# Kernel optimization log

Measured on AMD Instinct MI355X. Metric: run time of the kernel, lower is better.

## Reference

```python
import jax, jax.numpy as jnp
import numpy as np

K = 9  # 3x3 kernel field

def _conv(x, w, b, pad):
    out = jax.lax.conv_general_dilated(x, w, (1, 1), ((pad, pad), (pad, pad)),
                                       dimension_numbers=('NCHW', 'OIHW', 'NCHW'))
    return out + b[None, :, None, None]

def _conv_transpose(x, w, b):
    # torch ConvTranspose2d(k=3, stride=2, padding=1, output_padding=1); w: [Cin, Cout, 3, 3]
    wk = jnp.flip(jnp.transpose(w, (1, 0, 2, 3)), axis=(2, 3))  # [Cout, Cin, 3, 3]
    out = jax.lax.conv_general_dilated(x, wk, (1, 1), ((1, 2), (1, 2)),
                                       lhs_dilation=(2, 2),
                                       dimension_numbers=('NCHW', 'OIHW', 'NCHW'))
    return out + b[None, :, None, None]

def _modulated_deform_conv(x, offset, mask, w, b):
    # x: [B,C,H,W], offset: [B,2K,H,W] (y,x interleaved per kernel point, row-major),
    # mask: [B,K,H,W], w: [O,C,3,3]; stride=1, pad=1, dilation=1
    B, C, H, W = x.shape
    O = w.shape[0]
    off = offset.reshape(B, K, 2, H, W)
    ky, kx = jnp.meshgrid(jnp.arange(3), jnp.arange(3), indexing='ij')
    base_y = (jnp.arange(H)[None, :, None] - 1 + ky.reshape(K, 1, 1)).astype(x.dtype)  # [K,H,1]
    base_x = (jnp.arange(W)[None, None, :] - 1 + kx.reshape(K, 1, 1)).astype(x.dtype)  # [K,1,W]
    py = off[:, :, 0] + base_y[None]  # [B,K,H,W]
    px = off[:, :, 1] + base_x[None]
    y0 = jnp.floor(py); x0 = jnp.floor(px)
    wy = py - y0; wx = px - x0
    y0i = y0.astype(jnp.int32); x0i = x0.astype(jnp.int32)
    flat = x.reshape(B, C, H * W)

    def gather(yi, xi):
        valid = ((yi >= 0) & (yi < H) & (xi >= 0) & (xi < W)).astype(x.dtype)
        idx = jnp.clip(yi, 0, H - 1) * W + jnp.clip(xi, 0, W - 1)  # [B,K,H,W]
        g = jax.vmap(lambda im, ix: im[:, ix])(flat, idx.reshape(B, -1))  # [B,C,K*H*W]
        return g.reshape(B, C, K, H, W) * valid[:, None]

    v = (gather(y0i, x0i)         * ((1 - wy) * (1 - wx))[:, None]
       + gather(y0i, x0i + 1)     * ((1 - wy) * wx)[:, None]
       + gather(y0i + 1, x0i)     * (wy * (1 - wx))[:, None]
       + gather(y0i + 1, x0i + 1) * (wy * wx)[:, None])
    v = v * mask[:, None]  # modulation
    out = jnp.einsum('bckhw,ock->bohw', v, w.reshape(O, C, K))
    return out + b[None, :, None, None]

def setup_inputs() -> dict:
    key = jax.random.key(0)
    ks = jax.random.split(key, 8)
    B, Cin, Cout, H, W = 4, 128, 64, 64, 64
    return {
        'high_feature': jax.random.normal(ks[0], (B, Cin, H, W), jnp.float32),
        'low_feature': jax.random.normal(ks[1], (B, Cout, 2 * H, 2 * W), jnp.float32),
        'w_up': jax.random.normal(ks[2], (Cin, Cout, 3, 3), jnp.float32) * 0.03,
        'b_up': jnp.zeros((Cout,), jnp.float32),
        'w_off': jax.random.normal(ks[3], (3 * K, 2 * Cout, 3, 3), jnp.float32) * 0.02,
        'b_off': jnp.zeros((3 * K,), jnp.float32),
        'w_align': jax.random.normal(ks[4], (Cout, Cout, 3, 3), jnp.float32) * 0.04,
        'b_align': jnp.zeros((Cout,), jnp.float32),
    }

def reference(high_feature, low_feature, w_up, b_up, w_off, b_off, w_align, b_align):
    up = _conv_transpose(high_feature, w_up, b_up)            # [B,Cout,2H,2W]
    fo = _conv(jnp.concatenate([up, low_feature], axis=1), w_off, b_off, 1)
    offset, mask = fo[:, :2 * K], fo[:, 2 * K:]
    mask = 2.0 * jax.nn.sigmoid(mask)
    aligned = _modulated_deform_conv(up, offset, mask, w_align, b_align)
    aligned = jnp.where(aligned >= 0, aligned, 0.2 * aligned)  # LeakyReLU(0.2)
    return jnp.concatenate([aligned, low_feature], axis=1)
```

## Files before the change

kernel.cpp:

```cpp
#include <hip/hip_runtime.h>
#include <math.h>

namespace {
constexpr int B   = 4;
constexpr int CIN = 128;
constexpr int CO  = 64;
constexpr int HF  = 64;
constexpr int HO  = 128;
constexpr int HW  = HO * HO;
constexpr int NOFF = 27;

constexpr size_t UPB  = 0;
constexpr size_t LOB  = UPB + (size_t)B * HW * CO / 2;
constexpr size_t HBF  = LOB + (size_t)B * HW * CO / 2;
constexpr size_t WFRG = HBF + (size_t)B * HF * HF * CIN / 2;
constexpr size_t WFUP = WFRG + (size_t)(4 * 18 * 64 * 8) / 2;
constexpr size_t WFOF = WFUP + (size_t)(9 * 4 * 4 * 64 * 8) / 2;
}

using short8 = __attribute__((ext_vector_type(8))) short;
using f32x4  = __attribute__((ext_vector_type(4))) float;

__device__ __forceinline__ unsigned short f2bf(float f) {
  unsigned u = __float_as_uint(f);
  u += 0x7fffu + ((u >> 16) & 1u);
  return (unsigned short)(u >> 16);
}

__global__ void k_repack(const float* __restrict__ wup, const float* __restrict__ woff,
                         const float* __restrict__ wal, float* __restrict__ ws) {
  int i = blockIdx.x * 256 + threadIdx.x;
  if (i < 4 * 18 * 64 * 8) {
    int j = i & 7; int t2 = i >> 3;
    int lane = t2 & 63; int t3 = t2 >> 6;
    int kb = t3 % 18; int w = t3 / 18;
    int tap = kb >> 1;
    int c = (kb & 1) * 32 + ((lane >> 4) << 3) + j;
    int o = (w << 4) + (lane & 15);
    unsigned short* wfrag = (unsigned short*)(ws + WFRG);
    wfrag[i] = f2bf(wal[((size_t)o * CO + c) * 9 + tap]);
  }
  if (i < 9 * 4 * 4 * 64 * 8) {
    int j = i & 7; int lane = (i >> 3) & 63; int w = (i >> 9) & 3;
    int ch = (i >> 11) & 3; int rr = i >> 13;
    int c = ch * 32 + ((lane >> 4) << 3) + j;
    int o = w * 16 + (lane & 15);
    unsigned short* wfup = (unsigned short*)(ws + WFUP);
    wfup[i] = f2bf(wup[((size_t)c * CO + o) * 9 + rr]);
  }
  if (i < 9 * 4 * 2 * 64 * 8) {
    int j = i & 7; int lane = (i >> 3) & 63; int nt = (i >> 9) & 1;
    int kc = (i >> 10) & 3; int tap = i >> 12;
    int c = kc * 32 + ((lane >> 4) << 3) + j;
    int o = nt * 16 + (lane & 15);
    float v = 0.f;
    if (o < NOFF) v = woff[(((size_t)o * 2 * CO + c) * 3 + tap / 3) * 3 + (tap % 3)];
    unsigned short* wfo = (unsigned short*)(ws + WFOF);
    wfo[i] = f2bf(v);
  }
}

__global__ __launch_bounds__(256) void k_cvt(const float* __restrict__ high,
                                             float* __restrict__ ws) {
  __shared__ unsigned short tl[32][66];
  unsigned short* hbf = (unsigned short*)(ws + HBF);
  const int t = threadIdx.x;
  const int y = blockIdx.x, b = blockIdx.y;
  const int x = t & 63, clb = t >> 6;

  for (int c0 = 0; c0 < CIN; c0 += 32) {
    __syncthreads();
#pragma unroll
    for (int k = 0; k < 8; ++k) {
      int cl = clb * 8 + k;
      float v = high[(((size_t)b * CIN + c0 + cl) * HF + y) * HF + x];
      tl[cl][x] = f2bf(v);
    }
    __syncthreads();
    int px = t >> 2, cg = t & 3;
    ushort4 a, bb;
    a.x = tl[cg * 8 + 0][px]; a.y = tl[cg * 8 + 1][px];
    a.z = tl[cg * 8 + 2][px]; a.w = tl[cg * 8 + 3][px];
    bb.x = tl[cg * 8 + 4][px]; bb.y = tl[cg * 8 + 5][px];
    bb.z = tl[cg * 8 + 6][px]; bb.w = tl[cg * 8 + 7][px];
    unsigned short* dst = hbf + (((size_t)b * HF + y) * HF + px) * CIN + c0 + cg * 8;
    *(ushort4*)(dst) = a;
    *(ushort4*)(dst + 4) = bb;
  }
}

__global__ __launch_bounds__(256) void k_cvt2(const float* __restrict__ low,
                                              float* __restrict__ out,
                                              float* __restrict__ ws) {
  __shared__ unsigned short tl[64][130];
  unsigned short* lob = (unsigned short*)(ws + LOB);
  const int t = threadIdx.x;
  const int y = blockIdx.x, b = blockIdx.y;

#pragma unroll
  for (int it = 0; it < 8; ++it) {
    int i = it * 256 + t;
    int c = i >> 5, xi = (i & 31) * 4;
    float4 v = *(const float4*)(low + (((size_t)b * CO + c) * HO + y) * HO + xi);
    *(float4*)(out + (((size_t)b * 2 * CO + CO + c) * HO + y) * HO + xi) = v;
    tl[c][xi + 0] = f2bf(v.x); tl[c][xi + 1] = f2bf(v.y);
    tl[c][xi + 2] = f2bf(v.z); tl[c][xi + 3] = f2bf(v.w);
  }
  __syncthreads();
#pragma unroll
  for (int it = 0; it < 4; ++it) {
    int i = it * 256 + t;
    int x = i >> 3, cg = i & 7;
    unsigned rw[4];
#pragma unroll
    for (int p = 0; p < 4; ++p)
      rw[p] = (unsigned)tl[cg * 8 + 2 * p][x] | ((unsigned)tl[cg * 8 + 2 * p + 1][x] << 16);
    *(uint4*)(lob + (((size_t)b * HO + y) * HO + x) * CO + cg * 8) =
        make_uint4(rw[0], rw[1], rw[2], rw[3]);
  }
}

union SmemUp {
  unsigned short At[2][4][85][8];
  float accs[4][16][65];
};

__global__ __launch_bounds__(256) void k_up(const float* __restrict__ bup,
                                            float* __restrict__ ws) {
  __shared__ SmemUp sm;
  const unsigned short* hbf = (const unsigned short*)(ws + HBF);
  const uint4* wfu = (const uint4*)(ws + WFUP);
  unsigned short* upb = (unsigned short*)(ws + UPB);

  const int t    = threadIdx.x;
  const int lane = t & 63;
  const int oq   = __builtin_amdgcn_readfirstlane(t >> 6);
  const int z    = blockIdx.z;
  const int b    = z >> 2;
  const int pyv  = (z >> 1) & 1, pxv = z & 1;
  const int ty   = blockIdx.y * 4;
  const int tx   = blockIdx.x * 16;
  const int nty  = pyv + 1, ntx = pxv + 1;

  uint4 s0, s1;
  const int pxA = t >> 2, cgA = t & 3;
  const int i2 = t + 256, pxB = i2 >> 2, cgB = i2 & 3;

  auto load_chunk = [&](int c0) {
    {
      int gy = ty + pxA / 17, gx = tx + pxA % 17;
      s0 = make_uint4(0, 0, 0, 0);
      if (gy < HF && gx < HF)
        s0 = *(const uint4*)(hbf + (((size_t)b * HF + gy) * HF + gx) * CIN + c0 + cgA * 8);
    }
    s1 = make_uint4(0, 0, 0, 0);
    if (pxB < 85) {
      int gy = ty + pxB / 17, gx = tx + pxB % 17;
      if (gy < HF && gx < HF)
        s1 = *(const uint4*)(hbf + (((size_t)b * HF + gy) * HF + gx) * CIN + c0 + cgB * 8);
    }
  };
  auto write_chunk = [&](int buf) {
    *(uint4*)&sm.At[buf][cgA][pxA][0] = s0;
    if (pxB < 85) *(uint4*)&sm.At[buf][cgB][pxB][0] = s1;
  };

  f32x4 acc[4];
#pragma unroll
  for (int mt = 0; mt < 4; ++mt) acc[mt] = {0.f, 0.f, 0.f, 0.f};

  load_chunk(0);
  write_chunk(0);
  __syncthreads();

  union Cvt { uint4 u; short8 s; };
  int buf = 0;
#pragma unroll 1
  for (int ch = 0; ch < 4; ++ch) {
    if (ch < 3) load_chunk((ch + 1) * 32);
#pragma unroll
    for (int ti = 0; ti < 2; ++ti) {
      if (ti < nty) {
#pragma unroll
        for (int tj = 0; tj < 2; ++tj) {
          if (tj < ntx) {
            int ryA = pyv ? 2 - 2 * ti : 1;
            int rxA = pxv ? 2 - 2 * tj : 1;
            int rr = ryA * 3 + rxA;
            Cvt bw; bw.u = wfu[(((size_t)rr * 4 + ch) * 4 + oq) * 64 + lane];
#pragma unroll
            for (int mt = 0; mt < 4; ++mt) {
              Cvt av;
              av.u = *(const uint4*)&sm.At[buf][lane >> 4][(mt + ti) * 17 + (lane & 15) + tj][0];
              acc[mt] = __builtin_amdgcn_mfma_f32_16x16x32_bf16(av.s, bw.s, acc[mt], 0, 0, 0);
            }
          }
        }
      }
    }
    if (ch < 3) write_chunk(buf ^ 1);
    __syncthreads();
    buf ^= 1;
  }

#pragma unroll
  for (int mt = 0; mt < 4; ++mt)
#pragma unroll
    for (int r = 0; r < 4; ++r)
      sm.accs[oq][lane & 15][mt * 16 + (lane >> 4) * 4 + r] = acc[mt][r];
  __syncthreads();

  const int yo = 2 * (ty + (lane >> 4)) + pyv;
  const int xo = 2 * (tx + (lane & 15)) + pxv;
  unsigned short* dst = upb + (((size_t)b * HO + yo) * HO + xo) * CO + oq * 16;
  unsigned rw[8];
#pragma unroll
  for (int p = 0; p < 8; ++p) {
    float v0 = sm.accs[oq][2 * p][lane] + bup[oq * 16 + 2 * p];
    float v1 = sm.accs[oq][2 * p + 1][lane] + bup[oq * 16 + 2 * p + 1];
    rw[p] = (unsigned)f2bf(v0) | ((unsigned)f2bf(v1) << 16);
  }
  *(uint4*)dst = make_uint4(rw[0], rw[1], rw[2], rw[3]);
  *(uint4*)(dst + 8) = make_uint4(rw[4], rw[5], rw[6], rw[7]);
}

__global__ __launch_bounds__(256) void k_offdcn(const float* __restrict__ boff,
                                                const float* __restrict__ bal,
                                                float* __restrict__ out,
                                                const float* __restrict__ ws) {
  __shared__ float smem[9088];
  unsigned short* us_in = (unsigned short*)smem;
  float* fo_raw = smem;
  float* prm = smem + 2112;
  unsigned short* us_vt = (unsigned short*)(smem + 4992);

  const unsigned short* upb = (const unsigned short*)(ws + UPB);
  const unsigned short* lob = (const unsigned short*)(ws + LOB);
  const uint4* wfo = (const uint4*)(ws + WFOF);
  const uint4* wf  = (const uint4*)(ws + WFRG);

  const int t = threadIdx.x;
  const int lane = t & 63;
  const int w = __builtin_amdgcn_readfirstlane(t >> 6);
  const int mh = w >> 1, nt = w & 1;
  const int oq = w;
  const int b = blockIdx.z;
  const int tY = blockIdx.y * 4, tX = blockIdx.x * 16;
  const unsigned short* upB = upb + (size_t)b * HW * CO;

  union Cvt { uint4 u; short8 s; };

  for (int i = t; i < 16 * 108; i += 256) {
    int px = i >> 4, cg = i & 15;
    int gy = tY - 1 + px / 18, gx = tX - 1 + px % 18;
    uint4 v = make_uint4(0, 0, 0, 0);
    if (gy >= 0 && gy < HO && gx >= 0 && gx < HO) {
      const unsigned short* src =
          (cg < 8 ? upb : lob) + (((size_t)b * HO + gy) * HO + gx) * CO + (cg & 7) * 8;
      v = *(const uint4*)src;
    }
    *(uint4*)&us_in[((size_t)cg * 108 + px) * 8] = v;
  }
  __syncthreads();

  f32x4 acc2[2];
  acc2[0] = {0.f, 0.f, 0.f, 0.f}; acc2[1] = {0.f, 0.f, 0.f, 0.f};
#pragma unroll 1
  for (int tap = 0; tap < 9; ++tap) {
    int ky = tap / 3, kx = tap % 3;
#pragma unroll
    for (int kc = 0; kc < 4; ++kc) {
      Cvt bw; bw.u = wfo[(((size_t)tap * 4 + kc) * 2 + nt) * 64 + lane];
#pragma unroll
      for (int mt = 0; mt < 2; ++mt) {
        int sy = mh * 2 + mt;
        Cvt av;
        av.u = *(const uint4*)&us_in[(((size_t)(kc * 4 + (lane >> 4))) * 108 +
                                      (sy + ky) * 18 + (lane & 15) + kx) * 8];
        acc2[mt] = __builtin_amdgcn_mfma_f32_16x16x32_bf16(av.s, bw.s, acc2[mt], 0, 0, 0);
      }
    }
  }
  __syncthreads();

#pragma unroll
  for (int mt = 0; mt < 2; ++mt)
#pragma unroll
    for (int r = 0; r < 4; ++r)
      fo_raw[(nt * 16 + (lane & 15)) * 66 + mh * 32 + mt * 16 + (lane >> 4) * 4 + r] =
          acc2[mt][r];
  __syncthreads();

  for (int i = t; i < 9 * 64; i += 256) {
    int k = i >> 6, px = i & 63;
    int y = tY + (px >> 4), x = tX + (px & 15);
    float offy = fo_raw[(2 * k) * 66 + px] + boff[2 * k];
    float offx = fo_raw[(2 * k + 1) * 66 + px] + boff[2 * k + 1];
    float m = 2.f / (1.f + expf(-(fo_raw[(18 + k) * 66 + px] + boff[18 + k])));
    float pyf = offy + (float)(y - 1 + k / 3);
    float pxf = offx + (float)(x - 1 + k % 3);
    float y0f = floorf(pyf), x0f = floorf(pxf);
    float wy = pyf - y0f, wx = pxf - x0f;
    int y0 = (int)y0f, x0 = (int)x0f;
    int y1 = y0 + 1, x1 = x0 + 1;
    float vy0 = (y0 >= 0 && y0 < HO) ? m : 0.f;
    float vy1 = (y1 >= 0 && y1 < HO) ? m : 0.f;
    float vx0 = (x0 >= 0 && x0 < HO) ? 1.f : 0.f;
    float vx1 = (x1 >= 0 && x1 < HO) ? 1.f : 0.f;
    float* pr = prm + ((size_t)k * 64 + px) * 5;
    pr[0] = (1.f - wy) * (1.f - wx) * vy0 * vx0;
    pr[1] = (1.f - wy) * wx * vy0 * vx1;
    pr[2] = wy * (1.f - wx) * vy1 * vx0;
    pr[3] = wy * wx * vy1 * vx1;
    int cy0 = min(max(y0, 0), HO - 1), cy1 = min(max(y1, 0), HO - 1);
    int cx0 = min(max(x0, 0), HO - 1), cx1 = min(max(x1, 0), HO - 1);
    unsigned pc = (unsigned)cy0 | ((unsigned)cy1 << 8) |
                  ((unsigned)cx0 << 16) | ((unsigned)cx1 << 24);
    pr[4] = __uint_as_float(pc);
  }
  __syncthreads();

  uint4 u00[2], u01[2], u10[2], u11[2];

  auto issue = [&](int k) {
#pragma unroll
    for (int it = 0; it < 2; ++it) {
      int j = it * 256 + t;
      int q = j & 7, px = j >> 3;
      unsigned pc = __float_as_uint(prm[((size_t)k * 64 + px) * 5 + 4]);
      int cy0 = pc & 255, cy1 = (pc >> 8) & 255, cx0 = (pc >> 16) & 255, cx1 = pc >> 24;
      const unsigned short* base = upB + q * 8;
      u00[it] = *(const uint4*)(base + (size_t)(cy0 * HO + cx0) * CO);
      u01[it] = *(const uint4*)(base + (size_t)(cy0 * HO + cx1) * CO);
      u10[it] = *(const uint4*)(base + (size_t)(cy1 * HO + cx0) * CO);
      u11[it] = *(const uint4*)(base + (size_t)(cy1 * HO + cx1) * CO);
    }
  };

  auto combine = [&](int k, int buf) {
#pragma unroll
    for (int it = 0; it < 2; ++it) {
      int j = it * 256 + t;
      int q = j & 7, px = j >> 3;
      const float* pr = prm + ((size_t)k * 64 + px) * 5;
      float w0 = pr[0], w1 = pr[1], w2 = pr[2], w3 = pr[3];
      unsigned a0[4] = {u00[it].x, u00[it].y, u00[it].z, u00[it].w};
      unsigned a1[4] = {u01[it].x, u01[it].y, u01[it].z, u01[it].w};
      unsigned a2[4] = {u10[it].x, u10[it].y, u10[it].z, u10[it].w};
      unsigned a3[4] = {u11[it].x, u11[it].y, u11[it].z, u11[it].w};
      unsigned rw[4];
#pragma unroll
      for (int p = 0; p < 4; ++p) {
        float l0 = __uint_as_float(a0[p] << 16), h0 = __uint_as_float(a0[p] & 0xffff0000u);
        float l1 = __uint_as_float(a1[p] << 16), h1 = __uint_as_float(a1[p] & 0xffff0000u);
        float l2 = __uint_as_float(a2[p] << 16), h2 = __uint_as_float(a2[p] & 0xffff0000u);
        float l3 = __uint_as_float(a3[p] << 16), h3 = __uint_as_float(a3[p] & 0xffff0000u);
        float vlo = fmaf(w0, l0, fmaf(w1, l1, fmaf(w2, l2, w3 * l3)));
        float vhi = fmaf(w0, h0, fmaf(w1, h1, fmaf(w2, h2, w3 * h3)));
        rw[p] = (unsigned)f2bf(vlo) | ((unsigned)f2bf(vhi) << 16);
      }
      *(uint4*)&us_vt[(((size_t)buf * 8 + q) * 64 + px) * 8] = make_uint4(rw[0], rw[1], rw[2], rw[3]);
    }
  };

  f32x4 acc[4];
#pragma unroll
  for (int mt = 0; mt < 4; ++mt) acc[mt] = {0.f, 0.f, 0.f, 0.f};

  uint4 bw0 = wf[(oq * 18 + 0) * 64 + lane];
  uint4 bw1 = wf[(oq * 18 + 1) * 64 + lane];
  uint4 bn0, bn1;

  issue(0);
  combine(0, 0);
  __syncthreads();

  int buf = 0;
#pragma unroll 1
  for (int k = 0; k < 9; ++k) {
    if (k < 8) {
      issue(k + 1);
      bn0 = wf[(oq * 18 + 2 * k + 2) * 64 + lane];
      bn1 = wf[(oq * 18 + 2 * k + 3) * 64 + lane];
    }
#pragma unroll
    for (int kb2 = 0; kb2 < 2; ++kb2) {
      Cvt bfr; bfr.u = kb2 ? bw1 : bw0;
#pragma unroll
      for (int mt = 0; mt < 4; ++mt) {
        Cvt av;
        av.u = *(const uint4*)&us_vt[(((size_t)buf * 8 + kb2 * 4 + (lane >> 4)) * 64 +
                                      mt * 16 + (lane & 15)) * 8];
        acc[mt] = __builtin_amdgcn_mfma_f32_16x16x32_bf16(av.s, bfr.s, acc[mt], 0, 0, 0);
      }
    }
    if (k < 8) combine(k + 1, buf ^ 1);
    __syncthreads();
    bw0 = bn0; bw1 = bn1;
    buf ^= 1;
  }

  float* accs = smem;
#pragma unroll
  for (int mt = 0; mt < 4; ++mt)
#pragma unroll
    for (int r = 0; r < 4; ++r)
      accs[((size_t)oq * 16 + (lane & 15)) * 65 + mt * 16 + (lane >> 4) * 4 + r] = acc[mt][r];
  __syncthreads();

  const int y = tY + (lane >> 4), x = tX + (lane & 15);
  float* ob = out + (size_t)b * 2 * CO * HW + (size_t)y * HO + x;
#pragma unroll
  for (int ol = 0; ol < 16; ++ol) {
    int o = oq * 16 + ol;
    float v = accs[((size_t)oq * 16 + ol) * 65 + lane] + bal[o];
    v = (v >= 0.f) ? v : 0.2f * v;
    ob[(size_t)o * HW] = v;
  }
}

extern "C" void kernel_launch(void* const* d_in, const int* in_sizes, int n_in,
                              void* d_out, int out_size, void* d_ws, size_t ws_size,
                              hipStream_t stream) {
  const float* high = (const float*)d_in[0];
  const float* low  = (const float*)d_in[1];
  const float* wup  = (const float*)d_in[2];
  const float* bup  = (const float*)d_in[3];
  const float* woff = (const float*)d_in[4];
  const float* boff = (const float*)d_in[5];
  const float* wal  = (const float*)d_in[6];
  const float* bal  = (const float*)d_in[7];
  float* out = (float*)d_out;
  float* ws  = (float*)d_ws;

  k_repack<<<dim3(288), dim3(256), 0, stream>>>(wup, woff, wal, ws);
  k_cvt<<<dim3(HF, B), dim3(256), 0, stream>>>(high, ws);
  k_cvt2<<<dim3(HO, B), dim3(256), 0, stream>>>(low, out, ws);
  k_up<<<dim3(4, 16, B * 4), dim3(256), 0, stream>>>(bup, ws);
  k_offdcn<<<dim3(8, 32, B), dim3(256), 0, stream>>>(boff, bal, out, ws);
}
```

Before: 71.28 us.

## Merge prep kernels, swizzle block order for XCD locality, pack DCN params in bf16

Folds the weight repack and both layout-conversion kernels into one launch, with the work split by block-index ranges. This removes two kernel launches and the gaps between them. k_up and k_offdcn now use a 1D grid whose block index is remapped so that neighbouring tiles land on the same XCD (orig&7 interleave), which should improve L2 reuse. The bilinear weights in the deform-conv shared-memory parameters are packed as bf16 pairs, shrinking LDS from 9088 to 7936 floats to allow higher occupancy, at some cost in weight precision.

```diff
diff --git a/kernel.cpp b/kernel.cpp
--- a/kernel.cpp
+++ b/kernel.cpp
@@ -27,96 +27,103 @@
   return (unsigned short)(u >> 16);
 }
 
-__global__ void k_repack(const float* __restrict__ wup, const float* __restrict__ woff,
-                         const float* __restrict__ wal, float* __restrict__ ws) {
-  int i = blockIdx.x * 256 + threadIdx.x;
-  if (i < 4 * 18 * 64 * 8) {
-    int j = i & 7; int t2 = i >> 3;
-    int lane = t2 & 63; int t3 = t2 >> 6;
-    int kb = t3 % 18; int w = t3 / 18;
-    int tap = kb >> 1;
-    int c = (kb & 1) * 32 + ((lane >> 4) << 3) + j;
-    int o = (w << 4) + (lane & 15);
-    unsigned short* wfrag = (unsigned short*)(ws + WFRG);
-    wfrag[i] = f2bf(wal[((size_t)o * CO + c) * 9 + tap]);
-  }
-  if (i < 9 * 4 * 4 * 64 * 8) {
-    int j = i & 7; int lane = (i >> 3) & 63; int w = (i >> 9) & 3;
-    int ch = (i >> 11) & 3; int rr = i >> 13;
-    int c = ch * 32 + ((lane >> 4) << 3) + j;
-    int o = w * 16 + (lane & 15);
-    unsigned short* wfup = (unsigned short*)(ws + WFUP);
-    wfup[i] = f2bf(wup[((size_t)c * CO + o) * 9 + rr]);
-  }
-  if (i < 9 * 4 * 2 * 64 * 8) {
-    int j = i & 7; int lane = (i >> 3) & 63; int nt = (i >> 9) & 1;
-    int kc = (i >> 10) & 3; int tap = i >> 12;
-    int c = kc * 32 + ((lane >> 4) << 3) + j;
-    int o = nt * 16 + (lane & 15);
-    float v = 0.f;
-    if (o < NOFF) v = woff[(((size_t)o * 2 * CO + c) * 3 + tap / 3) * 3 + (tap % 3)];
-    unsigned short* wfo = (unsigned short*)(ws + WFOF);
-    wfo[i] = f2bf(v);
-  }
-}
-
-__global__ __launch_bounds__(256) void k_cvt(const float* __restrict__ high,
-                                             float* __restrict__ ws) {
-  __shared__ unsigned short tl[32][66];
-  unsigned short* hbf = (unsigned short*)(ws + HBF);
-  const int t = threadIdx.x;
-  const int y = blockIdx.x, b = blockIdx.y;
-  const int x = t & 63, clb = t >> 6;
-
-  for (int c0 = 0; c0 < CIN; c0 += 32) {
-    __syncthreads();
-#pragma unroll
-    for (int k = 0; k < 8; ++k) {
-      int cl = clb * 8 + k;
-      float v = high[(((size_t)b * CIN + c0 + cl) * HF + y) * HF + x];
-      tl[cl][x] = f2bf(v);
-    }
-    __syncthreads();
-    int px = t >> 2, cg = t & 3;
-    ushort4 a, bb;
-    a.x = tl[cg * 8 + 0][px]; a.y = tl[cg * 8 + 1][px];
-    a.z = tl[cg * 8 + 2][px]; a.w = tl[cg * 8 + 3][px];
-    bb.x = tl[cg * 8 + 4][px]; bb.y = tl[cg * 8 + 5][px];
-    bb.z = tl[cg * 8 + 6][px]; bb.w = tl[cg * 8 + 7][px];
-    unsigned short* dst = hbf + (((size_t)b * HF + y) * HF + px) * CIN + c0 + cg * 8;
-    *(ushort4*)(dst) = a;
-    *(ushort4*)(dst + 4) = bb;
-  }
-}
-
-__global__ __launch_bounds__(256) void k_cvt2(const float* __restrict__ low,
+__global__ __launch_bounds__(256) void k_prep(const float* __restrict__ high,
+                                              const float* __restrict__ low,
+                                              const float* __restrict__ wup,
+                                              const float* __restrict__ woff,
+                                              const float* __restrict__ wal,
                                               float* __restrict__ out,
                                               float* __restrict__ ws) {
   __shared__ unsigned short tl[64][130];
-  unsigned short* lob = (unsigned short*)(ws + LOB);
+  const int bid = blockIdx.x;
   const int t = threadIdx.x;
-  const int y = blockIdx.x, b = blockIdx.y;
-
-#pragma unroll
-  for (int it = 0; it < 8; ++it) {
-    int i = it * 256 + t;
-    int c = i >> 5, xi = (i & 31) * 4;
-    float4 v = *(const float4*)(low + (((size_t)b * CO + c) * HO + y) * HO + xi);
-    *(float4*)(out + (((size_t)b * 2 * CO + CO + c) * HO + y) * HO + xi) = v;
-    tl[c][xi + 0] = f2bf(v.x); tl[c][xi + 1] = f2bf(v.y);
-    tl[c][xi + 2] = f2bf(v.z); tl[c][xi + 3] = f2bf(v.w);
-  }
-  __syncthreads();
-#pragma unroll
-  for (int it = 0; it < 4; ++it) {
-    int i = it * 256 + t;
-    int x = i >> 3, cg = i & 7;
-    unsigned rw[4];
-#pragma unroll
-    for (int p = 0; p < 4; ++p)
-      rw[p] = (unsigned)tl[cg * 8 + 2 * p][x] | ((unsigned)tl[cg * 8 + 2 * p + 1][x] << 16);
-    *(uint4*)(lob + (((size_t)b * HO + y) * HO + x) * CO + cg * 8) =
-        make_uint4(rw[0], rw[1], rw[2], rw[3]);
+
+  if (bid < 288) {
+    int i = bid * 256 + t;
+    if (i < 4 * 18 * 64 * 8) {
+      int j = i & 7; int t2 = i >> 3;
+      int lane = t2 & 63; int t3 = t2 >> 6;
+      int kb = t3 % 18; int w = t3 / 18;
+      int tap = kb >> 1;
+      int c = (kb & 1) * 32 + ((lane >> 4) << 3) + j;
+      int o = (w << 4) + (lane & 15);
+      unsigned short* wfrag = (unsigned short*)(ws + WFRG);
+      wfrag[i] = f2bf(wal[((size_t)o * CO + c) * 9 + tap]);
+    }
+    if (i < 9 * 4 * 4 * 64 * 8) {
+      int j = i & 7; int lane = (i >> 3) & 63; int w = (i >> 9) & 3;
+      int ch = (i >> 11) & 3; int rr = i >> 13;
+      int c = ch * 32 + ((lane >> 4) << 3) + j;
+      int o = w * 16 + (lane & 15);
+      unsigned short* wfup = (unsigned short*)(ws + WFUP);
+      wfup[i] = f2bf(wup[((size_t)c * CO + o) * 9 + rr]);
+    }
+    if (i < 9 * 4 * 2 * 64 * 8) {
+      int j = i & 7; int lane = (i >> 3) & 63; int nt = (i >> 9) & 1;
+      int kc = (i >> 10) & 3; int tap = i >> 12;
+      int c = kc * 32 + ((lane >> 4) << 3) + j;
+      int o = nt * 16 + (lane & 15);
+      float v = 0.f;
+      if (o < NOFF) v = woff[(((size_t)o * 2 * CO + c) * 3 + tap / 3) * 3 + (tap % 3)];
+      unsigned short* wfo = (unsigned short*)(ws + WFOF);
+      wfo[i] = f2bf(v);
+    }
+    return;
+  }
+
+  if (bid < 544) {
+    unsigned short (*tl2)[66] = (unsigned short(*)[66])&tl[0][0];
+    unsigned short* hbf = (unsigned short*)(ws + HBF);
+    int j = bid - 288;
+    const int y = j & 63, b = j >> 6;
+    const int x = t & 63, clb = t >> 6;
+    for (int c0 = 0; c0 < CIN; c0 += 32) {
+      __syncthreads();
+#pragma unroll
+      for (int k = 0; k < 8; ++k) {
+        int cl = clb * 8 + k;
+        float v = high[(((size_t)b * CIN + c0 + cl) * HF + y) * HF + x];
+        tl2[cl][x] = f2bf(v);
+      }
+      __syncthreads();
+      int px = t >> 2, cg = t & 3;
+      ushort4 a, bb;
+      a.x = tl2[cg * 8 + 0][px]; a.y = tl2[cg * 8 + 1][px];
+      a.z = tl2[cg * 8 + 2][px]; a.w = tl2[cg * 8 + 3][px];
+      bb.x = tl2[cg * 8 + 4][px]; bb.y = tl2[cg * 8 + 5][px];
+      bb.z = tl2[cg * 8 + 6][px]; bb.w = tl2[cg * 8 + 7][px];
+      unsigned short* dst = hbf + (((size_t)b * HF + y) * HF + px) * CIN + c0 + cg * 8;
+      *(ushort4*)(dst) = a;
+      *(ushort4*)(dst + 4) = bb;
+    }
+    return;
+  }
+
+  {
+    unsigned short* lob = (unsigned short*)(ws + LOB);
+    int j = bid - 544;
+    const int y = j & 127, b = j >> 7;
+#pragma unroll
+    for (int it = 0; it < 8; ++it) {
+      int i = it * 256 + t;
+      int c = i >> 5, xi = (i & 31) * 4;
+      float4 v = *(const float4*)(low + (((size_t)b * CO + c) * HO + y) * HO + xi);
+      *(float4*)(out + (((size_t)b * 2 * CO + CO + c) * HO + y) * HO + xi) = v;
+      tl[c][xi + 0] = f2bf(v.x); tl[c][xi + 1] = f2bf(v.y);
+      tl[c][xi + 2] = f2bf(v.z); tl[c][xi + 3] = f2bf(v.w);
+    }
+    __syncthreads();
+#pragma unroll
+    for (int it = 0; it < 4; ++it) {
+      int i = it * 256 + t;
+      int x = i >> 3, cg = i & 7;
+      unsigned rw[4];
+#pragma unroll
+      for (int p = 0; p < 4; ++p)
+        rw[p] = (unsigned)tl[cg * 8 + 2 * p][x] | ((unsigned)tl[cg * 8 + 2 * p + 1][x] << 16);
+      *(uint4*)(lob + (((size_t)b * HO + y) * HO + x) * CO + cg * 8) =
+          make_uint4(rw[0], rw[1], rw[2], rw[3]);
+    }
   }
 }
 
@@ -135,11 +142,13 @@
   const int t    = threadIdx.x;
   const int lane = t & 63;
   const int oq   = __builtin_amdgcn_readfirstlane(t >> 6);
-  const int z    = blockIdx.z;
-  const int b    = z >> 2;
-  const int pyv  = (z >> 1) & 1, pxv = z & 1;
-  const int ty   = blockIdx.y * 4;
-  const int tx   = blockIdx.x * 16;
+  const int orig = blockIdx.x;
+  const int tile = ((orig & 7) << 7) + (orig >> 3);
+  const int par  = tile & 3;
+  const int pyv  = (par >> 1) & 1, pxv = par & 1;
+  const int tx   = ((tile >> 2) & 3) * 16;
+  const int ty   = ((tile >> 4) & 15) * 4;
+  const int b    = tile >> 8;
   const int nty  = pyv + 1, ntx = pxv + 1;
 
   uint4 s0, s1;
@@ -228,11 +237,11 @@
                                                 const float* __restrict__ bal,
                                                 float* __restrict__ out,
                                                 const float* __restrict__ ws) {
-  __shared__ float smem[9088];
+  __shared__ float smem[7936];
   unsigned short* us_in = (unsigned short*)smem;
   float* fo_raw = smem;
-  float* prm = smem + 2112;
-  unsigned short* us_vt = (unsigned short*)(smem + 4992);
+  unsigned* prm = (unsigned*)(smem + 2112);
+  unsigned short* us_vt = (unsigned short*)(smem + 3840);
 
   const unsigned short* upb = (const unsigned short*)(ws + UPB);
   const unsigned short* lob = (const unsigned short*)(ws + LOB);
@@ -244,8 +253,11 @@
   const int w = __builtin_amdgcn_readfirstlane(t >> 6);
   const int mh = w >> 1, nt = w & 1;
   const int oq = w;
-  const int b = blockIdx.z;
-  const int tY = blockIdx.y * 4, tX = blockIdx.x * 16;
+  const int orig = blockIdx.x;
+  const int tile = ((orig & 7) << 7) + (orig >> 3);
+  const int tX = (tile & 7) * 16;
+  const int tY = ((tile >> 3) & 31) * 4;
+  const int b  = tile >> 8;
   const unsigned short* upB = upb + (size_t)b * HW * CO;
 
   union Cvt { uint4 u; short8 s; };
@@ -307,16 +319,18 @@
     float vy1 = (y1 >= 0 && y1 < HO) ? m : 0.f;
     float vx0 = (x0 >= 0 && x0 < HO) ? 1.f : 0.f;
     float vx1 = (x1 >= 0 && x1 < HO) ? 1.f : 0.f;
-    float* pr = prm + ((size_t)k * 64 + px) * 5;
-    pr[0] = (1.f - wy) * (1.f - wx) * vy0 * vx0;
-    pr[1] = (1.f - wy) * wx * vy0 * vx1;
-    pr[2] = wy * (1.f - wx) * vy1 * vx0;
-    pr[3] = wy * wx * vy1 * vx1;
+    float w0 = (1.f - wy) * (1.f - wx) * vy0 * vx0;
+    float w1 = (1.f - wy) * wx * vy0 * vx1;
+    float w2 = wy * (1.f - wx) * vy1 * vx0;
+    float w3 = wy * wx * vy1 * vx1;
     int cy0 = min(max(y0, 0), HO - 1), cy1 = min(max(y1, 0), HO - 1);
     int cx0 = min(max(x0, 0), HO - 1), cx1 = min(max(x1, 0), HO - 1);
     unsigned pc = (unsigned)cy0 | ((unsigned)cy1 << 8) |
                   ((unsigned)cx0 << 16) | ((unsigned)cx1 << 24);
-    pr[4] = __uint_as_float(pc);
+    unsigned* pr = prm + ((size_t)k * 64 + px) * 3;
+    pr[0] = (unsigned)f2bf(w0) | ((unsigned)f2bf(w1) << 16);
+    pr[1] = (unsigned)f2bf(w2) | ((unsigned)f2bf(w3) << 16);
+    pr[2] = pc;
   }
   __syncthreads();
 
@@ -327,7 +341,7 @@
     for (int it = 0; it < 2; ++it) {
       int j = it * 256 + t;
       int q = j & 7, px = j >> 3;
-      unsigned pc = __float_as_uint(prm[((size_t)k * 64 + px) * 5 + 4]);
+      unsigned pc = prm[((size_t)k * 64 + px) * 3 + 2];
       int cy0 = pc & 255, cy1 = (pc >> 8) & 255, cx0 = (pc >> 16) & 255, cx1 = pc >> 24;
       const unsigned short* base = upB + q * 8;
       u00[it] = *(const uint4*)(base + (size_t)(cy0 * HO + cx0) * CO);
@@ -342,8 +356,10 @@
     for (int it = 0; it < 2; ++it) {
       int j = it * 256 + t;
       int q = j & 7, px = j >> 3;
-      const float* pr = prm + ((size_t)k * 64 + px) * 5;
-      float w0 = pr[0], w1 = pr[1], w2 = pr[2], w3 = pr[3];
+      const unsigned* pr = prm + ((size_t)k * 64 + px) * 3;
+      unsigned pw01 = pr[0], pw23 = pr[1];
+      float w0 = __uint_as_float(pw01 << 16), w1 = __uint_as_float(pw01 & 0xffff0000u);
+      float w2 = __uint_as_float(pw23 << 16), w3 = __uint_as_float(pw23 & 0xffff0000u);
       unsigned a0[4] = {u00[it].x, u00[it].y, u00[it].z, u00[it].w};
       unsigned a1[4] = {u01[it].x, u01[it].y, u01[it].z, u01[it].w};
       unsigned a2[4] = {u10[it].x, u10[it].y, u10[it].z, u10[it].w};
@@ -433,9 +449,7 @@
   float* out = (float*)d_out;
   float* ws  = (float*)d_ws;
 
-  k_repack<<<dim3(288), dim3(256), 0, stream>>>(wup, woff, wal, ws);
-  k_cvt<<<dim3(HF, B), dim3(256), 0, stream>>>(high, ws);
-  k_cvt2<<<dim3(HO, B), dim3(256), 0, stream>>>(low, out, ws);
-  k_up<<<dim3(4, 16, B * 4), dim3(256), 0, stream>>>(bup, ws);
-  k_offdcn<<<dim3(8, 32, B), dim3(256), 0, stream>>>(boff, bal, out, ws);
-}
+  k_prep<<<dim3(1056), dim3(256), 0, stream>>>(high, low, wup, woff, wal, out, ws);
+  k_up<<<dim3(1024), dim3(256), 0, stream>>>(bup, ws);
+  k_offdcn<<<dim3(1024), dim3(256), 0, stream>>>(boff, bal, out, ws);
+}
```

Result: faster. 64.23 us (-9.9%).
